# Optimization experiments

Hardware: AMD Instinct MI355X
Metric: run time of the kernel (lower is better)

## Reference

```python
import jax, jax.numpy as jnp
import numpy as np
from jax import lax

B, N, C, NP, NS, H, L = 2, 16384, 256, 2048, 32, 4, 2
DFF = 2 * C
RADIUS = 1.0
EPS = 1e-5


def setup_inputs() -> dict:
    key = jax.random.key(0)
    ks = jax.random.split(key, 12)
    s = 0.02
    f32 = jnp.float32
    return {
        "xyz": jax.random.normal(ks[0], (B, N, 3), f32),
        "features": jax.random.normal(ks[1], (B, C, N), f32),
        # positional encoding: Conv1x1(3->C/2)+BN(eval)+ReLU, Conv1x1(C/2->C)
        "pe1_w": jax.random.normal(ks[2], (C // 2, 3), f32) * s,
        "pe1_b": jnp.zeros((C // 2,), f32),
        "bn_g": jnp.ones((C // 2,), f32),
        "bn_b": jnp.zeros((C // 2,), f32),
        "bn_m": jnp.zeros((C // 2,), f32),
        "bn_v": jnp.ones((C // 2,), f32),
        "pe2_w": jax.random.normal(ks[3], (C, C // 2), f32) * s,
        "pe2_b": jnp.zeros((C,), f32),
        # L pre-norm transformer encoder layers (stacked on leading dim)
        "ipw": jax.random.normal(ks[4], (L, 3 * C, C), f32) * s,
        "ipb": jnp.zeros((L, 3 * C), f32),
        "opw": jax.random.normal(ks[5], (L, C, C), f32) * s,
        "opb": jnp.zeros((L, C), f32),
        "ln1s": jnp.ones((L, C), f32), "ln1b": jnp.zeros((L, C), f32),
        "ln2s": jnp.ones((L, C), f32), "ln2b": jnp.zeros((L, C), f32),
        "fc1w": jax.random.normal(ks[6], (L, DFF, C), f32) * s,
        "fc1b": jnp.zeros((L, DFF), f32),
        "fc2w": jax.random.normal(ks[7], (L, C, DFF), f32) * s,
        "fc2b": jnp.zeros((L, C), f32),
    }


def _fps(xyz, npoint):
    # D-FPS starting from point 0 (pointnet2 convention). xyz: [B,N,3]
    b, n, _ = xyz.shape

    def step(carry, _):
        dists, far = carry
        centroid = jnp.take_along_axis(xyz, far[:, None, None], axis=1)  # [B,1,3]
        d = jnp.sum((xyz - centroid) ** 2, -1)
        dists = jnp.minimum(dists, d)
        return (dists, jnp.argmax(dists, -1).astype(jnp.int32)), far

    init = (jnp.full((b, n), 1e10, jnp.float32), jnp.zeros((b,), jnp.int32))
    _, idx = lax.scan(step, init, None, length=npoint)
    return idx.T  # [B, npoint]


def _ball_query(xyz, new_xyz, radius, ns):
    # first <=ns points within radius, padded with the first hit. [B,NP,NS]
    n = xyz.shape[1]
    d2 = jnp.sum((new_xyz[:, :, None, :] - xyz[:, None, :, :]) ** 2, -1)  # [B,NP,N]
    scores = jnp.where(d2 < radius * radius, jnp.arange(n, dtype=jnp.int32), n)
    svals = jnp.sort(scores, axis=-1)[..., :ns]
    order = jnp.argsort(scores, axis=-1)[..., :ns].astype(jnp.int32)
    valid = svals < n
    return jnp.where(valid, order, order[..., :1])


def _ln(x, s, b):
    m = jnp.mean(x, -1, keepdims=True)
    v = jnp.var(x, -1, keepdims=True)
    return (x - m) * lax.rsqrt(v + EPS) * s + b


def _mha(x, w, bias, ow, ob):
    # x: [S, Bn, D] (seq-first, like nn.MultiheadAttention)
    S, Bn, D = x.shape
    hd = D // H
    qkv = x @ w.T + bias
    q, k, v = jnp.split(qkv, 3, -1)
    rs = lambda t: t.reshape(S, Bn, H, hd).transpose(1, 2, 0, 3)  # [Bn,H,S,hd]
    q, k, v = rs(q), rs(k), rs(v)
    att = jax.nn.softmax(jnp.einsum('bhqd,bhkd->bhqk', q, k) * (1.0 / np.sqrt(hd)), -1)
    o = jnp.einsum('bhqk,bhkd->bhqd', att, v).transpose(2, 0, 1, 3).reshape(S, Bn, D)
    return o @ ow.T + ob


def reference(xyz, features, pe1_w, pe1_b, bn_g, bn_b, bn_m, bn_v, pe2_w, pe2_b,
              ipw, ipb, opw, opb, ln1s, ln1b, ln2s, ln2b, fc1w, fc1b, fc2w, fc2b):
    # --- sample + group ---
    fps_idx = _fps(lax.stop_gradient(xyz), NP)                       # [B,NP]
    new_xyz = jnp.take_along_axis(xyz, fps_idx[:, :, None], axis=1)  # [B,NP,3]
    idx = _ball_query(lax.stop_gradient(xyz), lax.stop_gradient(new_xyz), RADIUS, NS)
    g_xyz = jax.vmap(lambda p, i: p[i])(xyz, idx) - new_xyz[:, :, None, :]  # [B,NP,NS,3]
    g_xyz = g_xyz.transpose(0, 3, 1, 2)                              # [B,3,NP,NS]
    g_feat = jax.vmap(lambda f, i: f[:, i])(features, idx)           # [B,C,NP,NS]
    # --- positional encoding (conv1x1 + BN(eval) + ReLU, conv1x1) ---
    h = jnp.einsum('oc,bcps->bops', pe1_w, g_xyz) + pe1_b[None, :, None, None]
    h = (h - bn_m[None, :, None, None]) * lax.rsqrt(bn_v + EPS)[None, :, None, None]
    h = jax.nn.relu(h * bn_g[None, :, None, None] + bn_b[None, :, None, None])
    pe = jnp.einsum('oc,bcps->bops', pe2_w, h) + pe2_b[None, :, None, None]
    x = g_feat + pe                                                  # [B,C,NP,NS]
    # --- local transformer over each neighborhood (seq len = NS) ---
    x = x.transpose(0, 2, 1, 3).reshape(B * NP, C, NS).transpose(2, 0, 1)  # [NS,B*NP,C]
    for l in range(L):
        x = _ln(x, ln1s[l], ln1b[l])
        x = x + _mha(x, ipw[l], ipb[l], opw[l], opb[l])
        x = _ln(x, ln2s[l], ln2b[l])
        x = x + jax.nn.relu(x @ fc1w[l].T + fc1b[l]) @ fc2w[l].T + fc2b[l]
    tf = x.transpose(1, 2, 0).reshape(B, NP, C, NS).transpose(0, 2, 1, 3)  # [B,C,NP,NS]
    Lf = NP * NS

    def scat(feat_b, tf_b, idx_b):
        idx_f = idx_b.reshape(-1)          # [Lf]
        ff = tf_b.reshape(C, -1)           # [C,Lf]
        pos = jnp.arange(Lf, dtype=jnp.int32)
        first = jax.ops.segment_min(pos, idx_f, num_segments=N)  # [N], maxint if absent
        valid = first < Lf
        safe = jnp.where(valid, first, 0)
        return jnp.where(valid[None, :], ff[:, safe], feat_b)    # [C,N]

    out = jax.vmap(scat)(features, tf, idx)  # [B,C,N]
    return out.transpose(0, 2, 1)            # [B,N,C]
```

## Files before the change

### kernel.cpp

```cpp
#include <hip/hip_runtime.h>

#define NB 2
#define NN 16384
#define NC 256
#define NPp 2048
#define NSs 32
#define NH 4
#define HDh 64
#define NL 2
#define NDFF 512
#define LFv (NPp*NSs)
#define LNEPS 1e-5f
#define NBLK 256
#define NTHR 512
#define NW 8
#define NQ 4
#define CHUNK (NN/NQ)

typedef short s16x8 __attribute__((ext_vector_type(8)));
typedef float f32x4 __attribute__((ext_vector_type(4)));
typedef float f32x2 __attribute__((ext_vector_type(2)));
typedef unsigned short u16;
typedef unsigned long long u64;

struct CtlBlock { int ctr1; int ctr2; int bar; };

__device__ __forceinline__ u16 f2bf(float f){
  unsigned u = __float_as_uint(f);
  u += 0x7fffu + ((u>>16)&1u);
  return (u16)(u>>16);
}

__device__ __forceinline__ f32x4 mfma16(s16x8 a, s16x8 b, f32x4 c){
  return __builtin_amdgcn_mfma_f32_16x16x32_bf16(a, b, c, 0, 0, 0);
}

__device__ __forceinline__ f32x2 pk_add(f32x2 a, f32x2 b){
  f32x2 d; asm("v_pk_add_f32 %0, %1, %2" : "=v"(d) : "v"(a), "v"(b)); return d;
}
__device__ __forceinline__ f32x2 pk_mul(f32x2 a, f32x2 b){
  f32x2 d; asm("v_pk_mul_f32 %0, %1, %2" : "=v"(d) : "v"(a), "v"(b)); return d;
}

#define DPP_FMAX(v, ctrl) do { \
  int _iv = __float_as_int(v); \
  int _sh = __builtin_amdgcn_update_dpp(_iv, _iv, (ctrl), 0xF, 0xF, false); \
  (v) = fmaxf((v), __int_as_float(_sh)); \
} while(0)

struct SMem {
  u64  masks[256];
  u64  keybuf[4];
  float wvc[2][NW][4];
  float xs[32][260];
  u16  xn[32][264];
  u16  qb[32][776];
  u16  pb[NH][32][40];
  int  idx_sh[32];
  float gx_sh[32][3];
  int  misc[16];
  int  win[32];
};

__global__ void k_prep(const float* __restrict__ ipw, const float* __restrict__ opw,
                       const float* __restrict__ fc1w, const float* __restrict__ fc2w,
                       const float* __restrict__ pe2w,
                       const float* __restrict__ bng, const float* __restrict__ bnb,
                       const float* __restrict__ bnm, const float* __restrict__ bnv,
                       u16* ipwb, u16* opwb, u16* fc1wb, u16* fc2wb, u16* pe2wb,
                       float* bnsc, float* bnsh, int* first, u64* cx2, u64* slots,
                       CtlBlock* ctl){
  const int i0 = blockIdx.x*blockDim.x + threadIdx.x;
  const int stride = gridDim.x*blockDim.x;
  for (int i=i0; i<NL*768*NC; i+=stride) ipwb[i] = f2bf(ipw[i]);
  for (int i=i0; i<NL*NC*NC; i+=stride)  opwb[i] = f2bf(opw[i]);
  for (int i=i0; i<NL*NDFF*NC; i+=stride) fc1wb[i] = f2bf(fc1w[i]);
  for (int i=i0; i<NL*NC*NDFF; i+=stride) fc2wb[i] = f2bf(fc2w[i]);
  for (int i=i0; i<NC*128; i+=stride)    pe2wb[i] = f2bf(pe2w[i]);
  for (int i=i0; i<NB*NN; i+=stride)     first[i] = LFv;
  for (int i=i0; i<NB*NPp*3; i+=stride)  cx2[i] = 0ull;
  for (int i=i0; i<NB*NQ*2*5; i+=stride) slots[i] = 0ull;
  for (int i=i0; i<128; i+=stride){
    float sc = bng[i]*rsqrtf(bnv[i]+LNEPS);
    bnsc[i] = sc; bnsh[i] = bnb[i] - bnm[i]*sc;
  }
  if (i0 == 0){ ctl->ctr1 = 0; ctl->ctr2 = 0; ctl->bar = 0; }
}

__global__ __launch_bounds__(256) void k_featT(const float* __restrict__ feat,
                                               float* __restrict__ featT){
  __shared__ float T[32][33];
  const int b = blockIdx.y;
  const int n0 = blockIdx.x*32;
  const int t = threadIdx.x;
  const int tn = t & 31, tc = t >> 5;
  for (int cb=0; cb<NC; cb+=32){
    #pragma unroll
    for (int i=0;i<32;i+=8)
      T[tc+i][tn] = feat[((size_t)b*NC + cb+tc+i)*NN + n0+tn];
    __syncthreads();
    #pragma unroll
    for (int i=0;i<32;i+=8)
      featT[((size_t)b*NN + n0+tc+i)*NC + cb+tn] = T[tn][tc+i];
    __syncthreads();
  }
}

#define SELC(S) case S: scx = px2[(S)>>1][(S)&1]; scy = py2[(S)>>1][(S)&1]; scz = pz2[(S)>>1][(S)&1]; break;

__device__ void fps_run4(int b, int q, const float* __restrict__ xyz,
                         u64* __restrict__ cx2, u64* __restrict__ slots, SMem& sm){
#pragma clang fp contract(off)
  const int t = threadIdx.x;
  const int lane = t & 63, wid = t >> 6;
  const int wbase = wid*64;
  const float* xb = xyz + (size_t)b*NN*3;
  const int gbase = q*CHUNK;
  f32x2 px2[4], py2[4], pz2[4], dd2[4];
  #pragma unroll
  for (int m=0;m<4;m++){
    int i0 = gbase + t + (2*m)*NTHR, i1 = gbase + t + (2*m+1)*NTHR;
    px2[m] = f32x2{xb[i0*3],   xb[i1*3]};
    py2[m] = f32x2{xb[i0*3+1], xb[i1*3+1]};
    pz2[m] = f32x2{xb[i0*3+2], xb[i1*3+2]};
    dd2[m] = f32x2{1e10f, 1e10f};
  }
  if (t < 4) sm.keybuf[t] = 0ull;
  float ncx, ncy, ncz;
  {
    float wx = xb[0], wy = xb[1], wz = xb[2];
    ncx=-wx; ncy=-wy; ncz=-wz;
    if (t==0 && q==0){
      size_t p0 = (size_t)(b*NPp)*3;
      __hip_atomic_store(&cx2[p0+0], ((u64)__float_as_uint(wx)<<32)|1u, __ATOMIC_RELAXED, __HIP_MEMORY_SCOPE_AGENT);
      __hip_atomic_store(&cx2[p0+1], ((u64)__float_as_uint(wy)<<32)|1u, __ATOMIC_RELAXED, __HIP_MEMORY_SCOPE_AGENT);
      __hip_atomic_store(&cx2[p0+2], ((u64)__float_as_uint(wz)<<32)|1u, __ATOMIC_RELAXED, __HIP_MEMORY_SCOPE_AGENT);
    }
  }
  __syncthreads();
  for (int step=1; step<NPp; ++step){
    const f32x2 ncx2={ncx,ncx}, ncy2={ncy,ncy}, ncz2={ncz,ncz};
    float bestv = -1.f;
    #pragma unroll
    for (int m=0;m<4;m++){
      f32x2 dx = pk_add(px2[m], ncx2);
      f32x2 dy = pk_add(py2[m], ncy2);
      f32x2 dz = pk_add(pz2[m], ncz2);
      f32x2 s  = pk_add(pk_add(pk_mul(dx,dx), pk_mul(dy,dy)), pk_mul(dz,dz));
      dd2[m].x = fminf(dd2[m].x, s.x);
      dd2[m].y = fminf(dd2[m].y, s.y);
      bestv = fmaxf(fmaxf(bestv, dd2[m].x), dd2[m].y);
    }
    float M = bestv;
    DPP_FMAX(M, 0x111); DPP_FMAX(M, 0x112); DPP_FMAX(M, 0x114); DPP_FMAX(M, 0x118);
    DPP_FMAX(M, 0x142); DPP_FMAX(M, 0x143);
    const int Mi = __builtin_amdgcn_readlane(__float_as_int(M), 63);
    const float Ms = __int_as_float(Mi);
    u64 bs[8];
    #pragma unroll
    for (int m=0;m<4;m++){
      bs[2*m]   = __ballot(dd2[m].x == Ms);
      bs[2*m+1] = __ballot(dd2[m].y == Ms);
    }
    int lc = 0;
    #pragma unroll
    for (int s=7;s>=0;s--)
      if (bs[s]) lc = wbase + s*NTHR + (__ffsll(bs[s])-1);
    const int kb = step & 3, cb = step & 1;
    if (lane==0){
      u64 key = ((u64)(unsigned)Mi << 32) | (unsigned)(0x7fffffff - (gbase + lc));
      atomicMax(&sm.keybuf[kb], key);
    }
    {
      const int slot = lc >> 9;
      float scx=0.f, scy=0.f, scz=0.f;
      switch(slot){
        SELC(0) SELC(1) SELC(2) SELC(3) SELC(4) SELC(5) SELC(6) SELC(7)
        default: break;
      }
      if (t == (lc & (NTHR-1))){
        sm.wvc[cb][wid][0]=scx; sm.wvc[cb][wid][1]=scy; sm.wvc[cb][wid][2]=scz;
      }
    }
    __syncthreads();
    if (wid==0){
      const u64 kloc = sm.keybuf[kb];
      const int gidx = 0x7fffffff - (int)(unsigned)(kloc & 0xffffffffull);
      const int wv = ((gidx - gbase) & (NTHR-1)) >> 6;
      const float bx = sm.wvc[cb][wv][0];
      const float by = sm.wvc[cb][wv][1];
      const float bz = sm.wvc[cb][wv][2];
      const unsigned tag = (unsigned)step;
      u64 w0 = (kloc & 0xffffffff00000000ull) | tag;
      u64 w1 = ((kloc & 0xffffffffull) << 32) | tag;
      u64 w2 = ((u64)__float_as_uint(bx) << 32) | tag;
      u64 w3 = ((u64)__float_as_uint(by) << 32) | tag;
      u64 w4 = ((u64)__float_as_uint(bz) << 32) | tag;
      u64 wown = (lane==0)?w0 : (lane==1)?w1 : (lane==2)?w2 : (lane==3)?w3 : w4;
      u64* mybase = slots + (size_t)(((b*NQ + q)*2 + cb)*5);
      if (lane < 5)
        __hip_atomic_store(&mybase[lane], wown, __ATOMIC_RELAXED, __HIP_MEMORY_SCOPE_AGENT);
      unsigned vhi = 0;
      if (lane < 15){
        int pi = lane/5, wj = lane - pi*5;
        int peerq = pi + (pi >= q ? 1 : 0);
        u64* src = slots + (size_t)(((b*NQ + peerq)*2 + cb)*5 + wj);
        u64 v;
        do { v = __hip_atomic_load(src, __ATOMIC_RELAXED, __HIP_MEMORY_SCOPE_AGENT); }
        while ((unsigned)v != tag);
        vhi = (unsigned)(v >> 32);
      }
      u64 bk = kloc;
      unsigned fxb = __float_as_uint(bx), fyb = __float_as_uint(by), fzb = __float_as_uint(bz);
      #pragma unroll
      for (int pi=0; pi<3; pi++){
        unsigned mh = (unsigned)__builtin_amdgcn_readlane((int)vhi, pi*5+0);
        unsigned il = (unsigned)__builtin_amdgcn_readlane((int)vhi, pi*5+1);
        u64 kp = ((u64)mh << 32) | il;
        if (kp > bk){
          bk = kp;
          fxb = (unsigned)__builtin_amdgcn_readlane((int)vhi, pi*5+2);
          fyb = (unsigned)__builtin_amdgcn_readlane((int)vhi, pi*5+3);
          fzb = (unsigned)__builtin_amdgcn_readlane((int)vhi, pi*5+4);
        }
      }
      if (lane==0){
        sm.misc[8]  = (int)fxb;
        sm.misc[9]  = (int)fyb;
        sm.misc[10] = (int)fzb;
        sm.keybuf[(step+2) & 3] = 0ull;
        if (q==0){
          size_t pb3 = (size_t)(b*NPp + step)*3;
          __hip_atomic_store(&cx2[pb3+0], ((u64)fxb<<32)|1u, __ATOMIC_RELAXED, __HIP_MEMORY_SCOPE_AGENT);
          __hip_atomic_store(&cx2[pb3+1], ((u64)fyb<<32)|1u, __ATOMIC_RELAXED, __HIP_MEMORY_SCOPE_AGENT);
          __hip_atomic_store(&cx2[pb3+2], ((u64)fzb<<32)|1u, __ATOMIC_RELAXED, __HIP_MEMORY_SCOPE_AGENT);
        }
      }
    }
    __syncthreads();
    ncx = -__int_as_float(sm.misc[8]);
    ncy = -__int_as_float(sm.misc[9]);
    ncz = -__int_as_float(sm.misc[10]);
  }
}

__device__ void seq_ballq(const float* __restrict__ xb, float cx, float cy, float cz,
                          SMem& sm, int t, int lane, int wid){
#pragma clang fp contract(off)
  for (int it=0; it<32; ++it){
    int cid = wid*32 + it;
    int i = cid*64 + lane;
    float dx=xb[i*3]-cx, dy=xb[i*3+1]-cy, dz=xb[i*3+2]-cz;
    float d2=(dx*dx+dy*dy)+dz*dz;
    u64 m = __ballot(d2 < 1.0f);
    if (lane==0) sm.masks[cid] = m;
  }
  __syncthreads();
  if (wid==0){
    u64 mk[4]; int cnt=0;
    #pragma unroll
    for (int j=0;j<4;j++){ mk[j]=sm.masks[lane*4+j]; cnt += __popcll(mk[j]); }
    int inc = cnt;
    #pragma unroll
    for (int ofs=1; ofs<64; ofs<<=1){
      int v = __shfl_up(inc, ofs);
      if (lane >= ofs) inc += v;
    }
    int r = inc - cnt;
    int tot = __shfl(inc, 63);
    #pragma unroll
    for (int j=0;j<4;j++){
      u64 msk = mk[j];
      int base = (lane*4+j)*64;
      while (msk && r < NSs){
        int bpos = __ffsll(msk)-1;
        sm.idx_sh[r] = base + bpos;
        msk &= msk-1;
        ++r;
      }
      if (r >= NSs) break;
    }
    int cc = tot < NSs ? tot : NSs;
    int pv = (tot > 0) ? sm.idx_sh[0] : 0;
    if (lane < NSs && lane >= cc) sm.idx_sh[lane] = pv;
  }
  __syncthreads();
}

__device__ __forceinline__ void ln_block512(SMem& sm, const float* __restrict__ s_,
                                            const float* __restrict__ b_, int t){
  const int s = t >> 4, j = t & 15;
  float v[16];
  float sum = 0.f;
  #pragma unroll
  for (int k=0;k<16;k++){ v[k]=sm.xs[s][j*16+k]; sum += v[k]; }
  #pragma unroll
  for (int m=1;m<16;m<<=1) sum += __shfl_xor(sum, m);
  const float mean = sum * (1.f/256.f);
  float vs = 0.f;
  #pragma unroll
  for (int k=0;k<16;k++){ float d=v[k]-mean; vs += d*d; }
  #pragma unroll
  for (int m=1;m<16;m<<=1) vs += __shfl_xor(vs, m);
  const float rstd = rsqrtf(vs*(1.f/256.f) + LNEPS);
  #pragma unroll
  for (int k=0;k<16;k++){
    int c = j*16+k;
    float y = (v[k]-mean)*rstd*s_[c] + b_[c];
    sm.xs[s][c] = y;
    sm.xn[s][c] = f2bf(y);
  }
}

__device__ void seq_pe_tf(SMem& sm, int b, float ccx, float ccy, float ccz,
    const float* __restrict__ xyz, const float* __restrict__ features,
    const float* __restrict__ featT, int useT,
    const float* __restrict__ pe1w, const float* __restrict__ pe1b,
    const float* __restrict__ bnsc, const float* __restrict__ bnsh,
    const u16* __restrict__ pe2wb, const float* __restrict__ pe2b,
    const u16* __restrict__ ipwb, const float* __restrict__ ipb,
    const u16* __restrict__ opwb, const float* __restrict__ opb,
    const float* __restrict__ ln1s, const float* __restrict__ ln1b,
    const float* __restrict__ ln2s, const float* __restrict__ ln2b,
    const u16* __restrict__ fc1wb, const float* __restrict__ fc1b,
    const u16* __restrict__ fc2wb, const float* __restrict__ fc2b){
  const int t = threadIdx.x, lane = t & 63, wid = t >> 6;
  const int c15 = lane & 15, g4 = lane >> 4;

  if (t < 96){
    int s = t/3, d = t%3;
    float cd = (d==0) ? ccx : ((d==1) ? ccy : ccz);
    sm.gx_sh[s][d] = xyz[((size_t)b*NN + sm.idx_sh[s])*3 + d] - cd;
  }
  if (useT){
    for (int e=t; e<32*NC; e+=NTHR){
      int s=e>>8, c=e&255;
      sm.xs[s][c] = featT[((size_t)b*NN + sm.idx_sh[s])*NC + c];
    }
  } else {
    for (int e=t; e<32*NC; e+=NTHR){
      int s=e>>8, c=e&255;
      sm.xs[s][c] = features[((size_t)b*NC + c)*NN + sm.idx_sh[s]];
    }
  }
  __syncthreads();
  for (int i=t; i<32*128; i+=NTHR){
    int s = i >> 7, o = i & 127;
    float h = pe1w[o*3]*sm.gx_sh[s][0] + pe1w[o*3+1]*sm.gx_sh[s][1] + pe1w[o*3+2]*sm.gx_sh[s][2] + pe1b[o];
    h = h*bnsc[o] + bnsh[o];
    sm.xn[s][o] = f2bf(h > 0.f ? h : 0.f);
  }
  __syncthreads();
  for (int tt=wid; tt<32; tt+=NW){
    int m0 = (tt & 1)*16, n0 = (tt >> 1)*16;
    f32x4 acc = {0.f,0.f,0.f,0.f};
    #pragma unroll
    for (int kk=0; kk<4; kk++){
      s16x8 a = *(const s16x8*)&sm.xn[m0+c15][kk*32 + g4*8];
      s16x8 bb = *(const s16x8*)&pe2wb[(size_t)(n0+c15)*128 + kk*32 + g4*8];
      acc = mfma16(a, bb, acc);
    }
    int col = n0 + c15;
    float bias = pe2b[col];
    #pragma unroll
    for (int r=0;r<4;r++) sm.xs[m0 + g4*4 + r][col] += acc[r] + bias;
  }
  __syncthreads();

  for (int l=0; l<NL; ++l){
    ln_block512(sm, ln1s + l*NC, ln1b + l*NC, t);
    __syncthreads();
    const u16* Wq = ipwb + (size_t)l*768*NC;
    const float* bq = ipb + l*768;
    for (int tt=wid; tt<96; tt+=NW){
      int m0 = (tt & 1)*16, n0 = (tt >> 1)*16;
      f32x4 acc = {0.f,0.f,0.f,0.f};
      #pragma unroll
      for (int kk=0;kk<8;kk++){
        s16x8 a = *(const s16x8*)&sm.xn[m0+c15][kk*32 + g4*8];
        s16x8 bb = *(const s16x8*)&Wq[(size_t)(n0+c15)*NC + kk*32 + g4*8];
        acc = mfma16(a, bb, acc);
      }
      int col = n0 + c15;
      float bias = bq[col];
      #pragma unroll
      for (int r=0;r<4;r++) sm.qb[m0 + g4*4 + r][col] = f2bf(acc[r] + bias);
    }
    __syncthreads();
    {
      const int h = wid & 3;
      const int mt = wid >> 2;
      f32x4 lac[2];
      #pragma unroll
      for (int nt=0;nt<2;nt++){
        f32x4 acc = {0.f,0.f,0.f,0.f};
        #pragma unroll
        for (int kk=0;kk<2;kk++){
          s16x8 a = *(const s16x8*)&sm.qb[mt*16+c15][h*HDh + kk*32 + g4*8];
          s16x8 bb = *(const s16x8*)&sm.qb[nt*16+c15][256 + h*HDh + kk*32 + g4*8];
          acc = mfma16(a, bb, acc);
        }
        lac[nt] = acc;
      }
      #pragma unroll
      for (int r=0;r<4;r++){
        float v0 = lac[0][r]*0.125f, v1 = lac[1][r]*0.125f;
        float mx = fmaxf(v0, v1);
        #pragma unroll
        for (int m=1;m<16;m<<=1) mx = fmaxf(mx, __shfl_xor(mx, m));
        float e0 = expf(v0-mx), e1 = expf(v1-mx);
        float smm = e0 + e1;
        #pragma unroll
        for (int m=1;m<16;m<<=1) smm += __shfl_xor(smm, m);
        float inv = 1.f/smm;
        int row = mt*16 + g4*4 + r;
        sm.pb[h][row][c15]    = f2bf(e0*inv);
        sm.pb[h][row][16+c15] = f2bf(e1*inv);
      }
      f32x4 oac[4];
      #pragma unroll
      for (int nt=0;nt<4;nt++){
        s16x8 bb;
        #pragma unroll
        for (int e=0;e<8;e++) bb[e] = (short)sm.qb[g4*8+e][512 + h*HDh + nt*16 + c15];
        f32x4 acc = {0.f,0.f,0.f,0.f};
        s16x8 a = *(const s16x8*)&sm.pb[h][mt*16+c15][g4*8];
        oac[nt] = mfma16(a, bb, acc);
      }
      __syncthreads();
      #pragma unroll
      for (int nt=0;nt<4;nt++)
        #pragma unroll
        for (int r=0;r<4;r++)
          sm.xn[mt*16 + g4*4 + r][h*HDh + nt*16 + c15] = f2bf(oac[nt][r]);
    }
    __syncthreads();
    const u16* Wo = opwb + (size_t)l*NC*NC;
    const float* bo = opb + l*NC;
    for (int tt=wid; tt<32; tt+=NW){
      int m0 = (tt & 1)*16, n0 = (tt >> 1)*16;
      f32x4 acc = {0.f,0.f,0.f,0.f};
      #pragma unroll
      for (int kk=0;kk<8;kk++){
        s16x8 a = *(const s16x8*)&sm.xn[m0+c15][kk*32 + g4*8];
        s16x8 bb = *(const s16x8*)&Wo[(size_t)(n0+c15)*NC + kk*32 + g4*8];
        acc = mfma16(a, bb, acc);
      }
      int col = n0 + c15;
      float bias = bo[col];
      #pragma unroll
      for (int r=0;r<4;r++) sm.xs[m0 + g4*4 + r][col] += acc[r] + bias;
    }
    __syncthreads();
    ln_block512(sm, ln2s + l*NC, ln2b + l*NC, t);
    __syncthreads();
    const u16* W1 = fc1wb + (size_t)l*NDFF*NC;
    for (int tt=wid; tt<64; tt+=NW){
      int m0 = (tt & 1)*16, n0 = (tt >> 1)*16;
      f32x4 acc = {0.f,0.f,0.f,0.f};
      #pragma unroll
      for (int kk=0;kk<8;kk++){
        s16x8 a = *(const s16x8*)&sm.xn[m0+c15][kk*32 + g4*8];
        s16x8 bb = *(const s16x8*)&W1[(size_t)(n0+c15)*NC + kk*32 + g4*8];
        acc = mfma16(a, bb, acc);
      }
      int col = n0 + c15;
      float bias = fc1b[l*NDFF + col];
      #pragma unroll
      for (int r=0;r<4;r++){
        float v = acc[r] + bias;
        sm.qb[m0 + g4*4 + r][col] = f2bf(v > 0.f ? v : 0.f);
      }
    }
    __syncthreads();
    const u16* W2 = fc2wb + (size_t)l*NC*NDFF;
    for (int tt=wid; tt<32; tt+=NW){
      int m0 = (tt & 1)*16, n0 = (tt >> 1)*16;
      f32x4 acc = {0.f,0.f,0.f,0.f};
      #pragma unroll
      for (int kk=0;kk<16;kk++){
        s16x8 a = *(const s16x8*)&sm.qb[m0+c15][kk*32 + g4*8];
        s16x8 bb = *(const s16x8*)&W2[(size_t)(n0+c15)*NDFF + kk*32 + g4*8];
        acc = mfma16(a, bb, acc);
      }
      int col = n0 + c15;
      float bias = fc2b[l*NC + col];
      #pragma unroll
      for (int r=0;r<4;r++) sm.xs[m0 + g4*4 + r][col] += acc[r] + bias;
    }
    __syncthreads();
  }
}

__global__ __launch_bounds__(NTHR, 2) void k_mega(
    const float* __restrict__ xyz, const float* __restrict__ features,
    const float* __restrict__ featT, int useT,
    u64* __restrict__ cx2, u64* __restrict__ slots, int* __restrict__ idxg,
    int* __restrict__ first, CtlBlock* ctl,
    const float* __restrict__ pe1w, const float* __restrict__ pe1b,
    const float* __restrict__ bnsc, const float* __restrict__ bnsh,
    const u16* __restrict__ pe2wb, const float* __restrict__ pe2b,
    const u16* __restrict__ ipwb, const float* __restrict__ ipb,
    const u16* __restrict__ opwb, const float* __restrict__ opb,
    const float* __restrict__ ln1s, const float* __restrict__ ln1b,
    const float* __restrict__ ln2s, const float* __restrict__ ln2b,
    const u16* __restrict__ fc1wb, const float* __restrict__ fc1b,
    const u16* __restrict__ fc2wb, const float* __restrict__ fc2b,
    float* __restrict__ out){
  __shared__ SMem sm;
  const int t = threadIdx.x, lane = t & 63, wid = t >> 6;
  const int bid = blockIdx.x;
  const int r8 = bid & 7;
  const bool isfps = (r8 < NB) && (bid < NQ*8);

  if (isfps){
    fps_run4(r8, bid >> 3, xyz, cx2, slots, sm);
  } else {
    for (;;){
      if (t==0) sm.misc[1] = atomicAdd(&ctl->ctr1, 1);
      __syncthreads();
      int p = sm.misc[1];
      if (p >= NB*NPp) break;
      int b = p >> 11, pp = p & (NPp-1);
      if (t==0){
        const u64* w = &cx2[(size_t)p*3];
        u64 w0, w1, w2;
        do { w0 = __hip_atomic_load(&w[0], __ATOMIC_RELAXED, __HIP_MEMORY_SCOPE_AGENT);
             if ((unsigned)w0 != 1u) __builtin_amdgcn_s_sleep(4);
        } while ((unsigned)w0 != 1u);
        do { w1 = __hip_atomic_load(&w[1], __ATOMIC_RELAXED, __HIP_MEMORY_SCOPE_AGENT); } while ((unsigned)w1 != 1u);
        do { w2 = __hip_atomic_load(&w[2], __ATOMIC_RELAXED, __HIP_MEMORY_SCOPE_AGENT); } while ((unsigned)w2 != 1u);
        sm.misc[4] = (int)(unsigned)(w0 >> 32);
        sm.misc[5] = (int)(unsigned)(w1 >> 32);
        sm.misc[6] = (int)(unsigned)(w2 >> 32);
      }
      __syncthreads();
      float cx = __int_as_float(sm.misc[4]);
      float cy = __int_as_float(sm.misc[5]);
      float cz = __int_as_float(sm.misc[6]);
      seq_ballq(xyz + (size_t)b*NN*3, cx, cy, cz, sm, t, lane, wid);
      if (t < NSs){
        atomicMin(&first[b*NN + sm.idx_sh[t]], pp*NSs + t);
        idxg[(size_t)p*NSs + t] = sm.idx_sh[t];
      }
      __syncthreads();
    }
  }

  __syncthreads();
  if (t==0){
    __builtin_amdgcn_fence(__ATOMIC_RELEASE, "agent");
    __hip_atomic_fetch_add(&ctl->bar, 1, __ATOMIC_RELAXED, __HIP_MEMORY_SCOPE_AGENT);
    while (__hip_atomic_load(&ctl->bar, __ATOMIC_RELAXED, __HIP_MEMORY_SCOPE_AGENT) < NBLK)
      __builtin_amdgcn_s_sleep(8);
    __builtin_amdgcn_fence(__ATOMIC_ACQUIRE, "agent");
  }
  __syncthreads();

  for (;;){
    if (t==0) sm.misc[1] = atomicAdd(&ctl->ctr2, 1);
    __syncthreads();
    int p = sm.misc[1];
    if (p >= NB*NPp) break;
    int b = p >> 11, pp = p & (NPp-1);
    if (t < NSs) sm.idx_sh[t] = idxg[(size_t)p*NSs + t];
    if (t==0) sm.misc[2] = 0;
    __syncthreads();
    if (t < NSs){
      int pos = pp*NSs + t;
      int f = first[b*NN + sm.idx_sh[t]];
      int w = (f == pos) ? 1 : 0;
      sm.win[t] = w;
      if (w) atomicOr(&sm.misc[2], 1);
    }
    __syncthreads();
    if (!sm.misc[2]) continue;
    u64 w0 = cx2[(size_t)p*3], w1 = cx2[(size_t)p*3+1], w2 = cx2[(size_t)p*3+2];
    float cx = __int_as_float((int)(unsigned)(w0 >> 32));
    float cy = __int_as_float((int)(unsigned)(w1 >> 32));
    float cz = __int_as_float((int)(unsigned)(w2 >> 32));
    seq_pe_tf(sm, b, cx, cy, cz, xyz, features, featT, useT,
              pe1w, pe1b, bnsc, bnsh, pe2wb, pe2b, ipwb, ipb, opwb, opb,
              ln1s, ln1b, ln2s, ln2b, fc1wb, fc1b, fc2wb, fc2b);
    for (int e=t; e<NSs*NC; e+=NTHR){
      int s = e >> 8, c = e & 255;
      if (sm.win[s]) out[((size_t)b*NN + sm.idx_sh[s])*NC + c] = sm.xs[s][c];
    }
    __syncthreads();
  }
}

__global__ __launch_bounds__(256) void k_outfill_T(const float* __restrict__ featT,
                                                   const int* __restrict__ first,
                                                   float* __restrict__ out){
  const int t = threadIdx.x;
  for (int rr=0; rr<8; ++rr){
    int row = blockIdx.x*8 + rr;
    if (first[row] == LFv)
      out[(size_t)row*NC + t] = featT[(size_t)row*NC + t];
  }
}

__global__ __launch_bounds__(256) void k_outfill_noT(const float* __restrict__ feat,
                                                     const int* __restrict__ first,
                                                     float* __restrict__ out){
  __shared__ float T[32][33];
  const int b = blockIdx.y;
  const int n0 = blockIdx.x*32;
  const int t = threadIdx.x;
  const int tn = t & 31, tc = t >> 5;
  for (int cb=0; cb<NC; cb+=32){
    #pragma unroll
    for (int i=0;i<32;i+=8)
      T[tc+i][tn] = feat[((size_t)b*NC + cb+tc+i)*NN + n0+tn];
    __syncthreads();
    #pragma unroll
    for (int i=0;i<32;i+=8){
      int n = n0 + tc + i;
      if (first[b*NN+n] == LFv)
        out[((size_t)b*NN + n)*NC + cb+tn] = T[tn][tc+i];
    }
    __syncthreads();
  }
}

extern "C" void kernel_launch(void* const* d_in, const int* in_sizes, int n_in,
                              void* d_out, int out_size, void* d_ws, size_t ws_size,
                              hipStream_t stream){
  const float* xyz   = (const float*)d_in[0];
  const float* feat  = (const float*)d_in[1];
  const float* pe1w  = (const float*)d_in[2];
  const float* pe1b  = (const float*)d_in[3];
  const float* bng   = (const float*)d_in[4];
  const float* bnb   = (const float*)d_in[5];
  const float* bnm   = (const float*)d_in[6];
  const float* bnv   = (const float*)d_in[7];
  const float* pe2w  = (const float*)d_in[8];
  const float* pe2b  = (const float*)d_in[9];
  const float* ipw   = (const float*)d_in[10];
  const float* ipb   = (const float*)d_in[11];
  const float* opw   = (const float*)d_in[12];
  const float* opb   = (const float*)d_in[13];
  const float* ln1s  = (const float*)d_in[14];
  const float* ln1b  = (const float*)d_in[15];
  const float* ln2s  = (const float*)d_in[16];
  const float* ln2b  = (const float*)d_in[17];
  const float* fc1w  = (const float*)d_in[18];
  const float* fc1b  = (const float*)d_in[19];
  const float* fc2w  = (const float*)d_in[20];
  const float* fc2b  = (const float*)d_in[21];
  float* out = (float*)d_out;

  char* ws = (char*)d_ws;
  size_t off = 0;
  auto alloc = [&](size_t bytes)->void*{
    void* p = ws + off;
    off = (off + bytes + 255) & ~(size_t)255;
    return p;
  };
  u64*   cx2     = (u64*)  alloc((size_t)NB*NPp*3*8);
  u64*   slots   = (u64*)  alloc((size_t)NB*NQ*2*5*8);
  int*   idxg    = (int*)  alloc((size_t)NB*NPp*NSs*4);
  int*   first   = (int*)  alloc((size_t)NB*NN*4);
  CtlBlock* ctl  = (CtlBlock*)alloc(sizeof(CtlBlock));
  float* bnsc    = (float*)alloc(128*4);
  float* bnsh    = (float*)alloc(128*4);
  u16*   ipwb    = (u16*)  alloc((size_t)NL*768*NC*2);
  u16*   opwb    = (u16*)  alloc((size_t)NL*NC*NC*2);
  u16*   fc1wb   = (u16*)  alloc((size_t)NL*NDFF*NC*2);
  u16*   fc2wb   = (u16*)  alloc((size_t)NL*NC*NDFF*2);
  u16*   pe2wb   = (u16*)  alloc((size_t)NC*128*2);
  int useT = (off + (size_t)NB*NN*NC*4 <= ws_size) ? 1 : 0;
  float* featT = (float*)(useT ? alloc((size_t)NB*NN*NC*4) : (void*)ws);

  k_prep<<<512, 256, 0, stream>>>(ipw, opw, fc1w, fc2w, pe2w, bng, bnb, bnm, bnv,
                                  ipwb, opwb, fc1wb, fc2wb, pe2wb, bnsc, bnsh,
                                  first, cx2, slots, ctl);
  if (useT)
    k_featT<<<dim3(NN/32, NB), 256, 0, stream>>>(feat, featT);

  const float* featT_c = featT;
  void* kargs[] = {
    (void*)&xyz, (void*)&feat, (void*)&featT_c, (void*)&useT,
    (void*)&cx2, (void*)&slots, (void*)&idxg, (void*)&first, (void*)&ctl,
    (void*)&pe1w, (void*)&pe1b, (void*)&bnsc, (void*)&bnsh,
    (void*)&pe2wb, (void*)&pe2b, (void*)&ipwb, (void*)&ipb,
    (void*)&opwb, (void*)&opb, (void*)&ln1s, (void*)&ln1b,
    (void*)&ln2s, (void*)&ln2b, (void*)&fc1wb, (void*)&fc1b,
    (void*)&fc2wb, (void*)&fc2b, (void*)&out };
  hipLaunchCooperativeKernel((void*)k_mega, dim3(NBLK), dim3(NTHR), kargs, 0, stream);

  if (useT)
    k_outfill_T<<<(NB*NN)/8, 256, 0, stream>>>(featT, first, out);
  else
    k_outfill_noT<<<dim3(NN/32, NB), 256, 0, stream>>>(feat, first, out);
  (void)in_sizes; (void)n_in; (void)out_size;
}
```

Baseline: 4.839 ms.

## Speculatively run transformer per group during FPS, halve FPS block split, commit winners after

FPS now splits each batch across 2 blocks instead of 4, doubling per-thread point registers and simplifying the cross-block exchange to a single peer with no second block barrier. When workspace permits, each group's transformer runs right after its ball query and overlaps with FPS, storing bf16 results for all groups instead of waiting for the first-occurrence phase. A new commit kernel gathers the winning rows or the original features. This removes the serialized second phase but computes every group, adds a large bf16 buffer, and rounds outputs to bf16.

After: 5.391 ms. 1.11x slower.

```diff
diff --git a/kernel.cpp b/kernel.cpp
--- a/kernel.cpp
+++ b/kernel.cpp
@@ -14,7 +14,7 @@
 #define NBLK 256
 #define NTHR 512
 #define NW 8
-#define NQ 4
+#define NQ 2
 #define CHUNK (NN/NQ)
 
 typedef short s16x8 __attribute__((ext_vector_type(8)));
@@ -108,7 +108,7 @@
 
 #define SELC(S) case S: scx = px2[(S)>>1][(S)&1]; scy = py2[(S)>>1][(S)&1]; scz = pz2[(S)>>1][(S)&1]; break;
 
-__device__ void fps_run4(int b, int q, const float* __restrict__ xyz,
+__device__ void fps_run2(int b, int q, const float* __restrict__ xyz,
                          u64* __restrict__ cx2, u64* __restrict__ slots, SMem& sm){
 #pragma clang fp contract(off)
   const int t = threadIdx.x;
@@ -116,9 +116,9 @@
   const int wbase = wid*64;
   const float* xb = xyz + (size_t)b*NN*3;
   const int gbase = q*CHUNK;
-  f32x2 px2[4], py2[4], pz2[4], dd2[4];
+  f32x2 px2[8], py2[8], pz2[8], dd2[8];
   #pragma unroll
-  for (int m=0;m<4;m++){
+  for (int m=0;m<8;m++){
     int i0 = gbase + t + (2*m)*NTHR, i1 = gbase + t + (2*m+1)*NTHR;
     px2[m] = f32x2{xb[i0*3],   xb[i1*3]};
     py2[m] = f32x2{xb[i0*3+1], xb[i1*3+1]};
@@ -142,7 +142,7 @@
     const f32x2 ncx2={ncx,ncx}, ncy2={ncy,ncy}, ncz2={ncz,ncz};
     float bestv = -1.f;
     #pragma unroll
-    for (int m=0;m<4;m++){
+    for (int m=0;m<8;m++){
       f32x2 dx = pk_add(px2[m], ncx2);
       f32x2 dy = pk_add(py2[m], ncy2);
       f32x2 dz = pk_add(pz2[m], ncz2);
@@ -156,15 +156,15 @@
     DPP_FMAX(M, 0x142); DPP_FMAX(M, 0x143);
     const int Mi = __builtin_amdgcn_readlane(__float_as_int(M), 63);
     const float Ms = __int_as_float(Mi);
-    u64 bs[8];
-    #pragma unroll
-    for (int m=0;m<4;m++){
+    u64 bs[16];
+    #pragma unroll
+    for (int m=0;m<8;m++){
       bs[2*m]   = __ballot(dd2[m].x == Ms);
       bs[2*m+1] = __ballot(dd2[m].y == Ms);
     }
     int lc = 0;
     #pragma unroll
-    for (int s=7;s>=0;s--)
+    for (int s=15;s>=0;s--)
       if (bs[s]) lc = wbase + s*NTHR + (__ffsll(bs[s])-1);
     const int kb = step & 3, cb = step & 1;
     if (lane==0){
@@ -176,6 +176,7 @@
       float scx=0.f, scy=0.f, scz=0.f;
       switch(slot){
         SELC(0) SELC(1) SELC(2) SELC(3) SELC(4) SELC(5) SELC(6) SELC(7)
+        SELC(8) SELC(9) SELC(10) SELC(11) SELC(12) SELC(13) SELC(14) SELC(15)
         default: break;
       }
       if (t == (lc & (NTHR-1))){
@@ -183,14 +184,14 @@
       }
     }
     __syncthreads();
-    if (wid==0){
-      const u64 kloc = sm.keybuf[kb];
-      const int gidx = 0x7fffffff - (int)(unsigned)(kloc & 0xffffffffull);
-      const int wv = ((gidx - gbase) & (NTHR-1)) >> 6;
-      const float bx = sm.wvc[cb][wv][0];
-      const float by = sm.wvc[cb][wv][1];
-      const float bz = sm.wvc[cb][wv][2];
-      const unsigned tag = (unsigned)step;
+    const u64 kloc = sm.keybuf[kb];
+    const int gidx = 0x7fffffff - (int)(unsigned)(kloc & 0xffffffffull);
+    const int wv = ((gidx - gbase) & (NTHR-1)) >> 6;
+    const float bx = sm.wvc[cb][wv][0];
+    const float by = sm.wvc[cb][wv][1];
+    const float bz = sm.wvc[cb][wv][2];
+    const unsigned tag = (unsigned)step;
+    if (wid==0 && lane<5){
       u64 w0 = (kloc & 0xffffffff00000000ull) | tag;
       u64 w1 = ((kloc & 0xffffffffull) << 32) | tag;
       u64 w2 = ((u64)__float_as_uint(bx) << 32) | tag;
@@ -198,49 +199,39 @@
       u64 w4 = ((u64)__float_as_uint(bz) << 32) | tag;
       u64 wown = (lane==0)?w0 : (lane==1)?w1 : (lane==2)?w2 : (lane==3)?w3 : w4;
       u64* mybase = slots + (size_t)(((b*NQ + q)*2 + cb)*5);
-      if (lane < 5)
-        __hip_atomic_store(&mybase[lane], wown, __ATOMIC_RELAXED, __HIP_MEMORY_SCOPE_AGENT);
-      unsigned vhi = 0;
-      if (lane < 15){
-        int pi = lane/5, wj = lane - pi*5;
-        int peerq = pi + (pi >= q ? 1 : 0);
-        u64* src = slots + (size_t)(((b*NQ + peerq)*2 + cb)*5 + wj);
-        u64 v;
-        do { v = __hip_atomic_load(src, __ATOMIC_RELAXED, __HIP_MEMORY_SCOPE_AGENT); }
-        while ((unsigned)v != tag);
-        vhi = (unsigned)(v >> 32);
-      }
-      u64 bk = kloc;
-      unsigned fxb = __float_as_uint(bx), fyb = __float_as_uint(by), fzb = __float_as_uint(bz);
-      #pragma unroll
-      for (int pi=0; pi<3; pi++){
-        unsigned mh = (unsigned)__builtin_amdgcn_readlane((int)vhi, pi*5+0);
-        unsigned il = (unsigned)__builtin_amdgcn_readlane((int)vhi, pi*5+1);
-        u64 kp = ((u64)mh << 32) | il;
-        if (kp > bk){
-          bk = kp;
-          fxb = (unsigned)__builtin_amdgcn_readlane((int)vhi, pi*5+2);
-          fyb = (unsigned)__builtin_amdgcn_readlane((int)vhi, pi*5+3);
-          fzb = (unsigned)__builtin_amdgcn_readlane((int)vhi, pi*5+4);
-        }
-      }
-      if (lane==0){
-        sm.misc[8]  = (int)fxb;
-        sm.misc[9]  = (int)fyb;
-        sm.misc[10] = (int)fzb;
-        sm.keybuf[(step+2) & 3] = 0ull;
-        if (q==0){
-          size_t pb3 = (size_t)(b*NPp + step)*3;
-          __hip_atomic_store(&cx2[pb3+0], ((u64)fxb<<32)|1u, __ATOMIC_RELAXED, __HIP_MEMORY_SCOPE_AGENT);
-          __hip_atomic_store(&cx2[pb3+1], ((u64)fyb<<32)|1u, __ATOMIC_RELAXED, __HIP_MEMORY_SCOPE_AGENT);
-          __hip_atomic_store(&cx2[pb3+2], ((u64)fzb<<32)|1u, __ATOMIC_RELAXED, __HIP_MEMORY_SCOPE_AGENT);
-        }
-      }
-    }
-    __syncthreads();
-    ncx = -__int_as_float(sm.misc[8]);
-    ncy = -__int_as_float(sm.misc[9]);
-    ncz = -__int_as_float(sm.misc[10]);
+      __hip_atomic_store(&mybase[lane], wown, __ATOMIC_RELAXED, __HIP_MEMORY_SCOPE_AGENT);
+    }
+    unsigned vhi = 0;
+    if (lane < 5){
+      u64* src = slots + (size_t)(((b*NQ + (q^1))*2 + cb)*5 + lane);
+      u64 v;
+      do { v = __hip_atomic_load(src, __ATOMIC_RELAXED, __HIP_MEMORY_SCOPE_AGENT); }
+      while ((unsigned)v != tag);
+      vhi = (unsigned)(v >> 32);
+    }
+    const unsigned mh = (unsigned)__builtin_amdgcn_readlane((int)vhi, 0);
+    const unsigned il = (unsigned)__builtin_amdgcn_readlane((int)vhi, 1);
+    const u64 kp = ((u64)mh << 32) | il;
+    unsigned fxb, fyb, fzb;
+    if (kp > kloc){
+      fxb = (unsigned)__builtin_amdgcn_readlane((int)vhi, 2);
+      fyb = (unsigned)__builtin_amdgcn_readlane((int)vhi, 3);
+      fzb = (unsigned)__builtin_amdgcn_readlane((int)vhi, 4);
+    } else {
+      fxb = __float_as_uint(bx); fyb = __float_as_uint(by); fzb = __float_as_uint(bz);
+    }
+    ncx = -__int_as_float((int)fxb);
+    ncy = -__int_as_float((int)fyb);
+    ncz = -__int_as_float((int)fzb);
+    if (t==0){
+      sm.keybuf[(step+2) & 3] = 0ull;
+      if (q==0){
+        size_t pb3 = (size_t)(b*NPp + step)*3;
+        __hip_atomic_store(&cx2[pb3+0], ((u64)fxb<<32)|1u, __ATOMIC_RELAXED, __HIP_MEMORY_SCOPE_AGENT);
+        __hip_atomic_store(&cx2[pb3+1], ((u64)fyb<<32)|1u, __ATOMIC_RELAXED, __HIP_MEMORY_SCOPE_AGENT);
+        __hip_atomic_store(&cx2[pb3+2], ((u64)fzb<<32)|1u, __ATOMIC_RELAXED, __HIP_MEMORY_SCOPE_AGENT);
+      }
+    }
   }
 }
 
@@ -494,7 +485,7 @@
 
 __global__ __launch_bounds__(NTHR, 2) void k_mega(
     const float* __restrict__ xyz, const float* __restrict__ features,
-    const float* __restrict__ featT, int useT,
+    const float* __restrict__ featT, int useT, u16* __restrict__ tfb, int spec,
     u64* __restrict__ cx2, u64* __restrict__ slots, int* __restrict__ idxg,
     int* __restrict__ first, CtlBlock* ctl,
     const float* __restrict__ pe1w, const float* __restrict__ pe1b,
@@ -510,12 +501,12 @@
   __shared__ SMem sm;
   const int t = threadIdx.x, lane = t & 63, wid = t >> 6;
   const int bid = blockIdx.x;
-  const int r8 = bid & 7;
-  const bool isfps = (r8 < NB) && (bid < NQ*8);
-
-  if (isfps){
-    fps_run4(r8, bid >> 3, xyz, cx2, slots, sm);
-  } else {
+  const bool isfps = ((bid & 7) < NB) && (bid < NQ*8);
+
+  if (isfps)
+    fps_run2(bid & 7, bid >> 3, xyz, cx2, slots, sm);
+
+  if (!isfps || spec){
     for (;;){
       if (t==0) sm.misc[1] = atomicAdd(&ctl->ctr1, 1);
       __syncthreads();
@@ -526,7 +517,7 @@
         const u64* w = &cx2[(size_t)p*3];
         u64 w0, w1, w2;
         do { w0 = __hip_atomic_load(&w[0], __ATOMIC_RELAXED, __HIP_MEMORY_SCOPE_AGENT);
-             if ((unsigned)w0 != 1u) __builtin_amdgcn_s_sleep(4);
+             if ((unsigned)w0 != 1u) __builtin_amdgcn_s_sleep(8);
         } while ((unsigned)w0 != 1u);
         do { w1 = __hip_atomic_load(&w[1], __ATOMIC_RELAXED, __HIP_MEMORY_SCOPE_AGENT); } while ((unsigned)w1 != 1u);
         do { w2 = __hip_atomic_load(&w[2], __ATOMIC_RELAXED, __HIP_MEMORY_SCOPE_AGENT); } while ((unsigned)w2 != 1u);
@@ -539,13 +530,20 @@
       float cy = __int_as_float(sm.misc[5]);
       float cz = __int_as_float(sm.misc[6]);
       seq_ballq(xyz + (size_t)b*NN*3, cx, cy, cz, sm, t, lane, wid);
-      if (t < NSs){
-        atomicMin(&first[b*NN + sm.idx_sh[t]], pp*NSs + t);
-        idxg[(size_t)p*NSs + t] = sm.idx_sh[t];
+      if (t < NSs) atomicMin(&first[b*NN + sm.idx_sh[t]], pp*NSs + t);
+      if (spec){
+        seq_pe_tf(sm, b, cx, cy, cz, xyz, features, featT, useT,
+                  pe1w, pe1b, bnsc, bnsh, pe2wb, pe2b, ipwb, ipb, opwb, opb,
+                  ln1s, ln1b, ln2s, ln2b, fc1wb, fc1b, fc2wb, fc2b);
+        for (int e=t; e<NSs*NC; e+=NTHR)
+          tfb[(size_t)p*NSs*NC + e] = f2bf(sm.xs[e>>8][e&255]);
+      } else {
+        if (t < NSs) idxg[(size_t)p*NSs + t] = sm.idx_sh[t];
       }
       __syncthreads();
     }
   }
+  if (spec) return;
 
   __syncthreads();
   if (t==0){
@@ -556,7 +554,6 @@
     __builtin_amdgcn_fence(__ATOMIC_ACQUIRE, "agent");
   }
   __syncthreads();
-
   for (;;){
     if (t==0) sm.misc[1] = atomicAdd(&ctl->ctr2, 1);
     __syncthreads();
@@ -587,6 +584,31 @@
       if (sm.win[s]) out[((size_t)b*NN + sm.idx_sh[s])*NC + c] = sm.xs[s][c];
     }
     __syncthreads();
+  }
+}
+
+__global__ __launch_bounds__(256) void k_commit(const u16* __restrict__ tfb,
+                                                const int* __restrict__ first,
+                                                const float* __restrict__ featT,
+                                                const float* __restrict__ feat,
+                                                int useT, float* __restrict__ out){
+  const int t = threadIdx.x;
+  const int row0 = blockIdx.x*16;
+  for (int r=0;r<16;++r){
+    int row = row0 + r;
+    int b = row >> 14;
+    int f = first[row];
+    float v;
+    if (f != LFv){
+      unsigned u = tfb[((size_t)b*NPp*NSs + f)*NC + t];
+      v = __int_as_float((int)(u << 16));
+    } else if (useT){
+      v = featT[(size_t)row*NC + t];
+    } else {
+      int n = row & (NN-1);
+      v = feat[((size_t)b*NC + t)*NN + n];
+    }
+    out[(size_t)row*NC + t] = v;
   }
 }
 
@@ -672,6 +694,8 @@
   u16*   pe2wb   = (u16*)  alloc((size_t)NC*128*2);
   int useT = (off + (size_t)NB*NN*NC*4 <= ws_size) ? 1 : 0;
   float* featT = (float*)(useT ? alloc((size_t)NB*NN*NC*4) : (void*)ws);
+  int spec = (off + (size_t)NB*NPp*NSs*NC*2 <= ws_size) ? 1 : 0;
+  u16* tfb = (u16*)(spec ? alloc((size_t)NB*NPp*NSs*NC*2) : (void*)ws);
 
   k_prep<<<512, 256, 0, stream>>>(ipw, opw, fc1w, fc2w, pe2w, bng, bnb, bnm, bnv,
                                   ipwb, opwb, fc1wb, fc2wb, pe2wb, bnsc, bnsh,
@@ -681,7 +705,7 @@
 
   const float* featT_c = featT;
   void* kargs[] = {
-    (void*)&xyz, (void*)&feat, (void*)&featT_c, (void*)&useT,
+    (void*)&xyz, (void*)&feat, (void*)&featT_c, (void*)&useT, (void*)&tfb, (void*)&spec,
     (void*)&cx2, (void*)&slots, (void*)&idxg, (void*)&first, (void*)&ctl,
     (void*)&pe1w, (void*)&pe1b, (void*)&bnsc, (void*)&bnsh,
     (void*)&pe2wb, (void*)&pe2b, (void*)&ipwb, (void*)&ipb,
@@ -690,9 +714,12 @@
     (void*)&fc2wb, (void*)&fc2b, (void*)&out };
   hipLaunchCooperativeKernel((void*)k_mega, dim3(NBLK), dim3(NTHR), kargs, 0, stream);
 
-  if (useT)
+  if (spec){
+    k_commit<<<(NB*NN)/16, 256, 0, stream>>>(tfb, first, featT, feat, useT, out);
+  } else if (useT){
     k_outfill_T<<<(NB*NN)/8, 256, 0, stream>>>(featT, first, out);
-  else
+  } else {
     k_outfill_noT<<<dim3(NN/32, NB), 256, 0, stream>>>(feat, first, out);
+  }
   (void)in_sizes; (void)n_in; (void)out_size;
 }
```
